# Kernel optimization log

Measured on AMD Instinct MI355X. Metric: run time of the kernel, lower is better.

Reference implementation:

```python
import jax, jax.numpy as jnp
import numpy as np

B, S, D, NH = 1, 2048, 2048, 8
DH = D // NH
BACKEND_EPS = 1e-6
NORM_EPS = 1e-6


def setup_inputs() -> dict:
    key = jax.random.key(0)
    ks = jax.random.split(key, 6)
    q = jax.random.normal(ks[0], (B, S, D), jnp.float32)
    k = jax.random.normal(ks[1], (B, S, D), jnp.float32)
    v = jax.random.normal(ks[2], (B, S, D), jnp.float32)
    igate_kernel = jax.random.normal(ks[3], (3 * D, NH), jnp.float32) * 0.02
    igate_bias = jax.random.normal(ks[4], (NH,), jnp.float32) * 0.1
    fgate_kernel = jax.random.normal(ks[5], (3 * D, NH), jnp.float32) * 0.02
    fgate_bias = jnp.linspace(3.0, 6.0, NH, dtype=jnp.float32)  # bias_linspace_init(3.0, 6.0)
    out_weight = jnp.ones((NH, DH), jnp.float32)  # MultiHeadLayerNorm scale (no bias)
    return dict(q=q, k=k, v=v, igate_kernel=igate_kernel, igate_bias=igate_bias,
                fgate_kernel=fgate_kernel, fgate_bias=fgate_bias, out_weight=out_weight)


def _mlstm_parallel_stabilized(q, k, v, i_pre, f_pre):
    # q,k,v: (B,NH,S,DH); i_pre,f_pre: (B,NH,S)
    s = q.shape[-2]
    dh = q.shape[-1]
    log_f = jax.nn.log_sigmoid(f_pre)                              # (B,NH,S)
    cum = jnp.pad(jnp.cumsum(log_f, axis=-1), ((0, 0), (0, 0), (1, 0)))  # (B,NH,S+1), cum[0]=0
    # logfg[t, s] = cum[t+1] - cum[s+1] = sum_{j=s+1}^{t} log_f[j], valid for s <= t
    logfg = cum[..., 1:, None] - cum[..., None, 1:]                # (B,NH,S,S)
    causal = jnp.tril(jnp.ones((s, s), dtype=bool))
    logfg = jnp.where(causal, logfg, -jnp.inf)
    log_D = logfg + i_pre[..., None, :]                            # add input gate at source position s
    m = jnp.max(log_D, axis=-1, keepdims=True)                     # stabilizer (B,NH,S,1)
    D = jnp.exp(log_D - m)
    qk = jnp.einsum('bhsd,bhtd->bhst', q, k) / jnp.sqrt(jnp.float32(dh))
    C = qk * D                                                     # (B,NH,S,S)
    n = jnp.maximum(jnp.abs(jnp.sum(C, axis=-1, keepdims=True)), jnp.exp(-m))
    return jnp.einsum('bhst,bhtd->bhsd', C / (n + BACKEND_EPS), v)


def reference(q, k, v, igate_kernel, igate_bias, fgate_kernel, fgate_bias, out_weight):
    qkv = jnp.concatenate([q, k, v], axis=-1)                      # (B,S,3D)
    i_pre = qkv @ igate_kernel + igate_bias                        # (B,S,NH)
    f_pre = qkv @ fgate_kernel + fgate_bias                        # (B,S,NH)
    qh = q.reshape(B, S, NH, DH).transpose(0, 2, 1, 3)             # (B,NH,S,DH)
    kh = k.reshape(B, S, NH, DH).transpose(0, 2, 1, 3)
    vh = v.reshape(B, S, NH, DH).transpose(0, 2, 1, 3)
    h = _mlstm_parallel_stabilized(qh, kh, vh,
                                   i_pre.transpose(0, 2, 1),
                                   f_pre.transpose(0, 2, 1))       # (B,NH,S,DH)
    h = h.transpose(0, 2, 1, 3)                                    # (B,S,NH,DH)
    mu = jnp.mean(h, axis=-1, keepdims=True)
    var = jnp.var(h, axis=-1, keepdims=True)
    hn = (h - mu) * jax.lax.rsqrt(var + NORM_EPS) * out_weight     # per-head LN, scale only
    return hn.reshape(B, S, D)
```

## Files before the change

kernel.cpp:

```cpp
#include <hip/hip_runtime.h>
#include <hip/hip_bf16.h>

#define SEQ 2048
#define DMODEL 2048
#define NHEAD 8
#define DHEAD 256

typedef _Float16 v8h __attribute__((ext_vector_type(8)));
typedef unsigned short v8u __attribute__((ext_vector_type(8)));
typedef float v4f __attribute__((ext_vector_type(4)));

__device__ __forceinline__ float b2f(unsigned short s) {
    return __uint_as_float(((unsigned)s) << 16);
}
__device__ __forceinline__ unsigned short f2b(float f) {
    unsigned u = __float_as_uint(f);
    u += 0x7fffu + ((u >> 16) & 1u);
    return (unsigned short)(u >> 16);
}
__device__ __forceinline__ unsigned short f2h(float f) {
    _Float16 h = (_Float16)f;
    return __builtin_bit_cast(unsigned short, h);
}
__device__ __forceinline__ float h2f(unsigned short s) {
    return (float)__builtin_bit_cast(_Float16, s);
}

__global__ __launch_bounds__(256) void k_detect(const unsigned short* q, int* flag) {
    __shared__ int cnt;
    if (threadIdx.x == 0) cnt = 0;
    __syncthreads();
    int wild = 0;
    for (int i = threadIdx.x; i < 2048; i += 256) {
        float x = b2f(q[i]);
        float ax = fabsf(x);
        if (!(ax <= 100.0f) || (x != 0.0f && ax < 1e-6f)) wild++;
    }
    atomicAdd(&cnt, wild);
    __syncthreads();
    if (threadIdx.x == 0) *flag = (cnt < 256) ? 1 : 0;
}

__global__ __launch_bounds__(256) void k_cvt_qk(const void* q, const void* k,
                                                const int* flag,
                                                unsigned short* qb, unsigned short* kb) {
    int bf = *(volatile const int*)flag;
    size_t i0 = ((size_t)blockIdx.x * 256 + threadIdx.x) * 8;
    v8u oq, ok;
    if (bf) {
        v8u uq = *(const v8u*)((const unsigned short*)q + i0);
        v8u uk = *(const v8u*)((const unsigned short*)k + i0);
#pragma unroll
        for (int j = 0; j < 8; j++) {
            oq[j] = f2h(b2f(uq[j]));
            ok[j] = f2h(b2f(uk[j]));
        }
    } else {
        const float* qf = (const float*)q;
        const float* kf = (const float*)k;
#pragma unroll
        for (int j = 0; j < 8; j++) {
            oq[j] = f2h(qf[i0 + j]);
            ok[j] = f2h(kf[i0 + j]);
        }
    }
    *(v8u*)(qb + i0) = oq;
    *(v8u*)(kb + i0) = ok;
}

__global__ __launch_bounds__(256) void k_cvt_gw(const void* ow, const int* flag, float* gw) {
    int bf = *(volatile const int*)flag;
    int i = blockIdx.x * 256 + threadIdx.x;
    gw[i] = bf ? b2f(((const unsigned short*)ow)[i]) : ((const float*)ow)[i];
}

__global__ __launch_bounds__(256) void k_tr_v(const void* v, const int* flag,
                                              unsigned short* vT) {
    __shared__ unsigned short tile[64][72];
    int bf = *(volatile const int*)flag;
    int s0 = blockIdx.x * 64, d0 = blockIdx.y * 64;
    int r = threadIdx.x >> 2, c0 = (threadIdx.x & 3) * 16;
    size_t base = (size_t)(s0 + r) * DMODEL + d0 + c0;
    if (bf) {
        const unsigned short* vp = (const unsigned short*)v;
        v8u a = *(const v8u*)(vp + base);
        v8u b = *(const v8u*)(vp + base + 8);
#pragma unroll
        for (int j = 0; j < 8; j++) { tile[r][c0 + j] = f2h(b2f(a[j])); tile[r][c0 + 8 + j] = f2h(b2f(b[j])); }
    } else {
        const float* vp = (const float*)v;
#pragma unroll
        for (int j = 0; j < 16; j++) tile[r][c0 + j] = f2h(vp[base + j]);
    }
    __syncthreads();
    int dr = threadIdx.x >> 2, sc0 = (threadIdx.x & 3) * 16;
    v8u o0, o1;
#pragma unroll
    for (int j = 0; j < 8; j++) { o0[j] = tile[sc0 + j][dr]; o1[j] = tile[sc0 + 8 + j][dr]; }
    int head = d0 >> 8;
    int dh = (d0 & 255) + dr;
    size_t ob = ((size_t)head * DHEAD + dh) * SEQ + s0 + sc0;
    *(v8u*)(vT + ob) = o0;
    *(v8u*)(vT + ob + 8) = o1;
}

__global__ __launch_bounds__(256) void k_gates(const void* q, const void* k, const void* v,
                                               const void* igk, const void* fgk,
                                               const int* flag, float* ipre, float* fpre) {
    __shared__ float x_lds[32][68];
    int bf = *(volatile const int*)flag;
    int s0 = blockIdx.x * 32;
    int c  = blockIdx.y;
    int tid = threadIdx.x;
    int sl = tid >> 3, hh = tid & 7;
    int rr = tid >> 3, j0 = (tid & 7) * 8;
    float accI = 0.f, accF = 0.f;
    for (int wd = 0; wd < 12; ++wd) {
        int gd0 = c * 768 + wd * 64;
        const void* src; int off;
        if (gd0 < 2048)      { src = q; off = gd0; }
        else if (gd0 < 4096) { src = k; off = gd0 - 2048; }
        else                 { src = v; off = gd0 - 4096; }
        __syncthreads();
        size_t base = (size_t)(s0 + rr) * DMODEL + off + j0;
        if (bf) {
            const unsigned short* sp = (const unsigned short*)src;
            v8u a = *(const v8u*)(sp + base);
#pragma unroll
            for (int j = 0; j < 8; j++) x_lds[rr][j0 + j] = b2f(a[j]);
        } else {
            const float* sp = (const float*)src;
#pragma unroll
            for (int j = 0; j < 8; j++) x_lds[rr][j0 + j] = sp[base + j];
        }
        __syncthreads();
        if (bf) {
            const unsigned short* ik = (const unsigned short*)igk;
            const unsigned short* fk = (const unsigned short*)fgk;
#pragma unroll 8
            for (int j = 0; j < 64; j++) {
                float x = x_lds[sl][j];
                int wi = (gd0 + j) * NHEAD + hh;
                accI += x * b2f(ik[wi]);
                accF += x * b2f(fk[wi]);
            }
        } else {
            const float* ik = (const float*)igk;
            const float* fk = (const float*)fgk;
#pragma unroll 8
            for (int j = 0; j < 64; j++) {
                float x = x_lds[sl][j];
                int wi = (gd0 + j) * NHEAD + hh;
                accI += x * ik[wi];
                accF += x * fk[wi];
            }
        }
    }
    atomicAdd(&ipre[hh * SEQ + s0 + sl], accI);
    atomicAdd(&fpre[hh * SEQ + s0 + sl], accF);
}

__global__ __launch_bounds__(256) void k_scan(const float* ipre, const float* fpre,
                                              const void* ib_, const void* fb_,
                                              const int* flag,
                                              float* a_g, float* amax_g, float* nfl_g) {
    __shared__ float sarr[256];
    int bf = *(volatile const int*)flag;
    int h = blockIdx.x, tid = threadIdx.x;
    float ib = bf ? b2f(((const unsigned short*)ib_)[h]) : ((const float*)ib_)[h];
    float fb = bf ? b2f(((const unsigned short*)fb_)[h]) : ((const float*)fb_)[h];
    int s0 = tid * 8;
    float lf[8], ip[8];
#pragma unroll
    for (int j = 0; j < 8; j++) {
        float fp = fpre[h * SEQ + s0 + j] + fb;
        lf[j] = fminf(fp, 0.0f) - log1pf(__expf(-fabsf(fp)));
        ip[j] = ipre[h * SEQ + s0 + j] + ib;
    }
    float cs[8]; float t = 0.f;
#pragma unroll
    for (int j = 0; j < 8; j++) { t += lf[j]; cs[j] = t; }
    sarr[tid] = t; __syncthreads();
    for (int ofs = 1; ofs < 256; ofs <<= 1) {
        float val = sarr[tid];
        if (tid >= ofs) val += sarr[tid - ofs];
        __syncthreads(); sarr[tid] = val; __syncthreads();
    }
    float excl = (tid > 0) ? sarr[tid - 1] : 0.0f;
    float cum[8], av[8];
#pragma unroll
    for (int j = 0; j < 8; j++) { cum[j] = excl + cs[j]; av[j] = ip[j] - cum[j]; }
    float mx = av[0];
#pragma unroll
    for (int j = 1; j < 8; j++) mx = fmaxf(mx, av[j]);
    __syncthreads(); sarr[tid] = mx; __syncthreads();
    for (int ofs = 1; ofs < 256; ofs <<= 1) {
        float val = sarr[tid];
        if (tid >= ofs) val = fmaxf(val, sarr[tid - ofs]);
        __syncthreads(); sarr[tid] = val; __syncthreads();
    }
    float run = (tid > 0) ? sarr[tid - 1] : -3.0e38f;
#pragma unroll
    for (int j = 0; j < 8; j++) {
        run = fmaxf(run, av[j]);
        int s = s0 + j;
        a_g[h * SEQ + s]    = av[j];
        amax_g[h * SEQ + s] = run;
        float m = cum[j] + run;
        nfl_g[h * SEQ + s]  = __expf(fminf(fmaxf(-m, -60.f), 60.f));
    }
}

__global__ __launch_bounds__(256) void k_main(const unsigned short* __restrict__ qb,
                                              const unsigned short* __restrict__ kb,
                                              const unsigned short* __restrict__ vT,
                                              const float* __restrict__ a_g,
                                              const float* __restrict__ amax_g,
                                              float* __restrict__ h_buf,
                                              float* __restrict__ rs_buf) {
    __shared__ __align__(16) unsigned short q_lds[32][264];
    __shared__ __align__(16) unsigned short k_lds[32][264];
    __shared__ __align__(16) unsigned short vT_lds[272][40];
    __shared__ __align__(16) unsigned short P_lds[32][40];
    __shared__ __align__(16) unsigned short Plo_lds[32][40];
    __shared__ float a_s[32], amax_t[32];

    const int h   = blockIdx.x;
    const int y   = blockIdx.y;
    const int tid = threadIdx.x;
    const int lane = tid & 63;
    const int w   = tid >> 6;
    const int l15 = lane & 15;
    const int qd  = (lane >> 4) & 3;
    const int hd0 = h * DHEAD;

    int u         = 65 * (y >> 1) + ((y & 1) ? 33 : 0);
    int remaining = (y & 1) ? 32 : 33;
    int tile = (int)((sqrtf(8.0f * (float)u + 1.0f) - 1.0f) * 0.5f);
    while ((tile + 1) * (tile + 2) / 2 <= u) ++tile;
    while (tile * (tile + 1) / 2 > u) --tile;
    int js = u - tile * (tile + 1) / 2;
    bool needQ = true;

    for (int i = tid; i < 16 * 40; i += 256) {
        int r2 = i / 40, c2 = i % 40;
        vT_lds[256 + r2][c2] = (r2 == 0 && c2 < 32) ? (unsigned short)0x3C00 : (unsigned short)0;
    }

    const v4f vzero = {0.f, 0.f, 0.f, 0.f};
    v4f acc[2][4];
    v4f accN[2];
#pragma unroll
    for (int m = 0; m < 2; m++) {
        accN[m] = vzero;
#pragma unroll
        for (int n = 0; n < 4; n++) acc[m][n] = vzero;
    }

    const int mw = w >> 1, nw = w & 1;
    const int krow = tid >> 3, kc0 = (tid & 7) * 32;

    v8u kr0, kr1, kr2, kr3, vr0, vr1, vr2, vr3;
    float areg = 0.f;
    {
        const int s0 = js * 32;
        const unsigned short* ks = kb + (size_t)(s0 + krow) * DMODEL + hd0 + kc0;
        kr0 = *(const v8u*)(ks);      kr1 = *(const v8u*)(ks + 8);
        kr2 = *(const v8u*)(ks + 16); kr3 = *(const v8u*)(ks + 24);
        const unsigned short* vs = vT + (size_t)(hd0 + tid) * SEQ + s0;
        vr0 = *(const v8u*)(vs);      vr1 = *(const v8u*)(vs + 8);
        vr2 = *(const v8u*)(vs + 16); vr3 = *(const v8u*)(vs + 24);
        if (tid < 32) areg = a_g[h * SEQ + s0 + tid];
    }

    for (;;) {
        const int t0 = tile * 32;
        __syncthreads();
        if (needQ) {
            const unsigned short* src = qb + (size_t)(t0 + krow) * DMODEL + hd0 + kc0;
#pragma unroll
            for (int i = 0; i < 4; i++)
                *(v8u*)&q_lds[krow][kc0 + i * 8] = *(const v8u*)(src + i * 8);
            if (tid < 32) amax_t[tid] = amax_g[h * SEQ + t0 + tid];
            needQ = false;
        }
        *(v8u*)&k_lds[krow][kc0]      = kr0;
        *(v8u*)&k_lds[krow][kc0 + 8]  = kr1;
        *(v8u*)&k_lds[krow][kc0 + 16] = kr2;
        *(v8u*)&k_lds[krow][kc0 + 24] = kr3;
        *(v8u*)&vT_lds[tid][0]  = vr0;
        *(v8u*)&vT_lds[tid][8]  = vr1;
        *(v8u*)&vT_lds[tid][16] = vr2;
        *(v8u*)&vT_lds[tid][24] = vr3;
        if (tid < 32) a_s[tid] = areg;
        __syncthreads();

        v4f c = vzero;
#pragma unroll
        for (int d0 = 0; d0 < 256; d0 += 32) {
            v8h a = *(const v8h*)&q_lds[mw * 16 + l15][d0 + qd * 8];
            v8h b = *(const v8h*)&k_lds[nw * 16 + l15][d0 + qd * 8];
            c = __builtin_amdgcn_mfma_f32_16x16x32_f16(a, b, c, 0, 0, 0);
        }
        {
            const bool diag = (js == tile);
            const int col = nw * 16 + l15;
            const float av = a_s[col];
#pragma unroll
            for (int r = 0; r < 4; r++) {
                int row = mw * 16 + qd * 4 + r;
                float arg = fminf(av - amax_t[row], 0.0f);
                float val = c[r] * 0.0625f * __expf(arg);
                if (diag && col > row) val = 0.0f;
                unsigned short hi = f2h(val);
                float lo = val - h2f(hi);
                P_lds[row][col]   = hi;
                Plo_lds[row][col] = f2h(lo);
            }
        }
        __syncthreads();

        int ntile = tile, njs = js + 1; bool nq = false;
        if (njs > tile) { ntile = tile + 1; njs = 0; nq = true; }
        if (remaining > 1) {
            const int s0 = njs * 32;
            const unsigned short* ks = kb + (size_t)(s0 + krow) * DMODEL + hd0 + kc0;
            kr0 = *(const v8u*)(ks);      kr1 = *(const v8u*)(ks + 8);
            kr2 = *(const v8u*)(ks + 16); kr3 = *(const v8u*)(ks + 24);
            const unsigned short* vs = vT + (size_t)(hd0 + tid) * SEQ + s0;
            vr0 = *(const v8u*)(vs);      vr1 = *(const v8u*)(vs + 8);
            vr2 = *(const v8u*)(vs + 16); vr3 = *(const v8u*)(vs + 24);
            if (tid < 32) areg = a_g[h * SEQ + s0 + tid];
        }

        v8h aH0 = *(const v8h*)&P_lds[l15][qd * 8];
        v8h aH1 = *(const v8h*)&P_lds[16 + l15][qd * 8];
        v8h aL0 = *(const v8h*)&Plo_lds[l15][qd * 8];
        v8h aL1 = *(const v8h*)&Plo_lds[16 + l15][qd * 8];
#pragma unroll
        for (int nn = 0; nn < 4; nn++) {
            v8h bV = *(const v8h*)&vT_lds[w * 64 + nn * 16 + l15][qd * 8];
            acc[0][nn] = __builtin_amdgcn_mfma_f32_16x16x32_f16(aH0, bV, acc[0][nn], 0, 0, 0);
            acc[0][nn] = __builtin_amdgcn_mfma_f32_16x16x32_f16(aL0, bV, acc[0][nn], 0, 0, 0);
            acc[1][nn] = __builtin_amdgcn_mfma_f32_16x16x32_f16(aH1, bV, acc[1][nn], 0, 0, 0);
            acc[1][nn] = __builtin_amdgcn_mfma_f32_16x16x32_f16(aL1, bV, acc[1][nn], 0, 0, 0);
        }
        if (w == 3) {
            v8h bN = *(const v8h*)&vT_lds[256 + l15][qd * 8];
            accN[0] = __builtin_amdgcn_mfma_f32_16x16x32_f16(aH0, bN, accN[0], 0, 0, 0);
            accN[0] = __builtin_amdgcn_mfma_f32_16x16x32_f16(aL0, bN, accN[0], 0, 0, 0);
            accN[1] = __builtin_amdgcn_mfma_f32_16x16x32_f16(aH1, bN, accN[1], 0, 0, 0);
            accN[1] = __builtin_amdgcn_mfma_f32_16x16x32_f16(aL1, bN, accN[1], 0, 0, 0);
        }

        if (js == tile || remaining == 1) {
#pragma unroll
            for (int m = 0; m < 2; m++)
#pragma unroll
                for (int r = 0; r < 4; r++) {
                    int row = t0 + m * 16 + qd * 4 + r;
#pragma unroll
                    for (int nn = 0; nn < 4; nn++) {
                        int col = hd0 + w * 64 + nn * 16 + l15;
                        atomicAdd(&h_buf[(size_t)row * DMODEL + col], acc[m][nn][r]);
                        acc[m][nn][r] = 0.f;
                    }
                    if (w == 3 && l15 == 0)
                        atomicAdd(&rs_buf[h * SEQ + row], accN[m][r]);
                    accN[m][r] = 0.f;
                }
        }
        if (--remaining == 0) break;
        tile = ntile; js = njs; needQ = nq;
    }
}

__global__ __launch_bounds__(256) void k_finish(const float* __restrict__ h_buf,
                                                const float* __restrict__ rs_buf,
                                                const float* __restrict__ nfl_g,
                                                const float* __restrict__ gw,
                                                const int* flag, void* out) {
    const int wv = threadIdx.x >> 6, lane = threadIdx.x & 63;
    const int rid = blockIdx.x * 4 + wv;
    const int s = rid >> 3, h = rid & 7;
    const int bf = *(volatile const int*)flag;
    float rs  = rs_buf[h * SEQ + s];
    float nfl = nfl_g[h * SEQ + s];
    float sc  = 1.0f / (fmaxf(fabsf(rs), nfl) + 1e-6f);
    size_t base = (size_t)s * DMODEL + h * DHEAD + lane * 4;
    v4f hv = *(const v4f*)(h_buf + base);
#pragma unroll
    for (int j = 0; j < 4; j++) hv[j] *= sc;
    float sm = hv[0] + hv[1] + hv[2] + hv[3];
    float sq = hv[0] * hv[0] + hv[1] * hv[1] + hv[2] * hv[2] + hv[3] * hv[3];
#pragma unroll
    for (int m = 1; m < 64; m <<= 1) {
        sm += __shfl_xor(sm, m, 64);
        sq += __shfl_xor(sq, m, 64);
    }
    float mean = sm * (1.0f / 256.0f);
    float var  = fmaxf(sq * (1.0f / 256.0f) - mean * mean, 0.0f);
    float rstd = rsqrtf(var + 1e-6f);
    const float* g = gw + h * DHEAD + lane * 4;
    if (bf) {
        unsigned short* o = (unsigned short*)out + base;
#pragma unroll
        for (int j = 0; j < 4; j++) o[j] = f2b((hv[j] - mean) * rstd * g[j]);
    } else {
        float* o = (float*)out + base;
#pragma unroll
        for (int j = 0; j < 4; j++) o[j] = (hv[j] - mean) * rstd * g[j];
    }
}

extern "C" void kernel_launch(void* const* d_in, const int* in_sizes, int n_in,
                              void* d_out, int out_size, void* d_ws, size_t ws_size,
                              hipStream_t stream) {
    const void* q   = d_in[0];
    const void* k   = d_in[1];
    const void* v   = d_in[2];
    const void* igk = d_in[3];
    const void* igb = d_in[4];
    const void* fgk = d_in[5];
    const void* fgb = d_in[6];
    const void* ow  = d_in[7];

    char* ws = (char*)d_ws;
    int*   flag   = (int*)(ws + 0);
    float* ipre   = (float*)(ws + 1024);
    float* fpre   = (float*)(ws + 1024 + 1 * 65536);
    float* a_g    = (float*)(ws + 1024 + 2 * 65536);
    float* amax_g = (float*)(ws + 1024 + 3 * 65536);
    float* nfl_g  = (float*)(ws + 1024 + 4 * 65536);
    float* gw     = (float*)(ws + 1024 + 5 * 65536);
    unsigned short* qb = (unsigned short*)(ws + 1024 + 5 * 65536 + 8192);
    unsigned short* kb = qb + (size_t)SEQ * DMODEL;
    unsigned short* vT = kb + (size_t)SEQ * DMODEL;
    float* rs_buf = (float*)((char*)vT + (size_t)SEQ * DMODEL * 2);
    float* h_buf  = (float*)((char*)rs_buf + 65536);

    hipMemsetAsync(ipre, 0, 2 * 65536, stream);
    hipMemsetAsync(rs_buf, 0, 65536 + (size_t)SEQ * DMODEL * 4, stream);
    k_detect<<<1, 256, 0, stream>>>((const unsigned short*)q, flag);
    k_cvt_qk<<<2048, 256, 0, stream>>>(q, k, flag, qb, kb);
    k_cvt_gw<<<8, 256, 0, stream>>>(ow, flag, gw);
    k_tr_v<<<dim3(32, 32), 256, 0, stream>>>(v, flag, vT);
    k_gates<<<dim3(64, 8), 256, 0, stream>>>(q, k, v, igk, fgk, flag, ipre, fpre);
    k_scan<<<8, 256, 0, stream>>>(ipre, fpre, igb, fgb, flag, a_g, amax_g, nfl_g);
    k_main<<<dim3(8, 64), 256, 0, stream>>>(qb, kb, vT, a_g, amax_g, h_buf, rs_buf);
    k_finish<<<4096, 256, 0, stream>>>(h_buf, rs_buf, nfl_g, gw, flag, d_out);
}
```

Measured before the change: 269.4 us.

## Fuse dtype detect, conversions, V transpose and gate projections into one pre-pass

Merges the detect, q/k conversion, V transpose and gate-projection kernels into a single k_pre kernel. Each block reads its slice of q/k/v once and uses it both to emit fp16 copies and to accumulate gate partial sums, which are written to per-slice partial buffers instead of atomics. k_scan then reduces the six partials, and k_finish reads the LN weight directly. This removes redundant global reads of q/k/v, several launches and one memset, in exchange for each block redoing the dtype detection and using only 384 blocks for the fused pre-pass.

```diff
diff --git a/kernel.cpp b/kernel.cpp
--- a/kernel.cpp
+++ b/kernel.cpp
@@ -26,141 +26,106 @@
     return (float)__builtin_bit_cast(_Float16, s);
 }
 
-__global__ __launch_bounds__(256) void k_detect(const unsigned short* q, int* flag) {
+__global__ __launch_bounds__(256) void k_pre(const void* q, const void* k, const void* v,
+                                             const void* igk, const void* fgk,
+                                             int* flag,
+                                             unsigned short* qb, unsigned short* kb,
+                                             unsigned short* vT,
+                                             float* iparts, float* fparts) {
+    __shared__ float x_lds[32][67];
     __shared__ int cnt;
-    if (threadIdx.x == 0) cnt = 0;
+    const int tid = threadIdx.x;
+
+    if (tid == 0) cnt = 0;
     __syncthreads();
-    int wild = 0;
-    for (int i = threadIdx.x; i < 2048; i += 256) {
-        float x = b2f(q[i]);
-        float ax = fabsf(x);
-        if (!(ax <= 100.0f) || (x != 0.0f && ax < 1e-6f)) wild++;
-    }
-    atomicAdd(&cnt, wild);
+    {
+        const unsigned short* qp = (const unsigned short*)q;
+        int wild = 0;
+        for (int i = tid; i < 2048; i += 256) {
+            float x = b2f(qp[i]);
+            float ax = fabsf(x);
+            if (!(ax <= 100.0f) || (x != 0.0f && ax < 1e-6f)) wild++;
+        }
+        atomicAdd(&cnt, wild);
+    }
     __syncthreads();
-    if (threadIdx.x == 0) *flag = (cnt < 256) ? 1 : 0;
-}
-
-__global__ __launch_bounds__(256) void k_cvt_qk(const void* q, const void* k,
-                                                const int* flag,
-                                                unsigned short* qb, unsigned short* kb) {
-    int bf = *(volatile const int*)flag;
-    size_t i0 = ((size_t)blockIdx.x * 256 + threadIdx.x) * 8;
-    v8u oq, ok;
-    if (bf) {
-        v8u uq = *(const v8u*)((const unsigned short*)q + i0);
-        v8u uk = *(const v8u*)((const unsigned short*)k + i0);
-#pragma unroll
-        for (int j = 0; j < 8; j++) {
-            oq[j] = f2h(b2f(uq[j]));
-            ok[j] = f2h(b2f(uk[j]));
-        }
-    } else {
-        const float* qf = (const float*)q;
-        const float* kf = (const float*)k;
-#pragma unroll
-        for (int j = 0; j < 8; j++) {
-            oq[j] = f2h(qf[i0 + j]);
-            ok[j] = f2h(kf[i0 + j]);
-        }
-    }
-    *(v8u*)(qb + i0) = oq;
-    *(v8u*)(kb + i0) = ok;
-}
-
-__global__ __launch_bounds__(256) void k_cvt_gw(const void* ow, const int* flag, float* gw) {
-    int bf = *(volatile const int*)flag;
-    int i = blockIdx.x * 256 + threadIdx.x;
-    gw[i] = bf ? b2f(((const unsigned short*)ow)[i]) : ((const float*)ow)[i];
-}
-
-__global__ __launch_bounds__(256) void k_tr_v(const void* v, const int* flag,
-                                              unsigned short* vT) {
-    __shared__ unsigned short tile[64][72];
-    int bf = *(volatile const int*)flag;
-    int s0 = blockIdx.x * 64, d0 = blockIdx.y * 64;
-    int r = threadIdx.x >> 2, c0 = (threadIdx.x & 3) * 16;
-    size_t base = (size_t)(s0 + r) * DMODEL + d0 + c0;
-    if (bf) {
-        const unsigned short* vp = (const unsigned short*)v;
-        v8u a = *(const v8u*)(vp + base);
-        v8u b = *(const v8u*)(vp + base + 8);
-#pragma unroll
-        for (int j = 0; j < 8; j++) { tile[r][c0 + j] = f2h(b2f(a[j])); tile[r][c0 + 8 + j] = f2h(b2f(b[j])); }
-    } else {
-        const float* vp = (const float*)v;
-#pragma unroll
-        for (int j = 0; j < 16; j++) tile[r][c0 + j] = f2h(vp[base + j]);
-    }
-    __syncthreads();
-    int dr = threadIdx.x >> 2, sc0 = (threadIdx.x & 3) * 16;
-    v8u o0, o1;
-#pragma unroll
-    for (int j = 0; j < 8; j++) { o0[j] = tile[sc0 + j][dr]; o1[j] = tile[sc0 + 8 + j][dr]; }
-    int head = d0 >> 8;
-    int dh = (d0 & 255) + dr;
-    size_t ob = ((size_t)head * DHEAD + dh) * SEQ + s0 + sc0;
-    *(v8u*)(vT + ob) = o0;
-    *(v8u*)(vT + ob + 8) = o1;
-}
-
-__global__ __launch_bounds__(256) void k_gates(const void* q, const void* k, const void* v,
-                                               const void* igk, const void* fgk,
-                                               const int* flag, float* ipre, float* fpre) {
-    __shared__ float x_lds[32][68];
-    int bf = *(volatile const int*)flag;
-    int s0 = blockIdx.x * 32;
-    int c  = blockIdx.y;
-    int tid = threadIdx.x;
-    int sl = tid >> 3, hh = tid & 7;
-    int rr = tid >> 3, j0 = (tid & 7) * 8;
+    const int bf = (cnt < 256) ? 1 : 0;
+    if (blockIdx.x == 0 && blockIdx.y == 0 && tid == 0) *flag = bf;
+
+    const int s0 = blockIdx.x * 32;
+    const int z  = blockIdx.y;
+    const int tz = z >> 1;
+    const int dbase = (z & 1) * 1024;
+    const void* src = (tz == 0) ? q : (tz == 1) ? k : v;
+    unsigned short* dst16 = (tz == 0) ? qb : kb;
+
+    const int r  = tid >> 3, c0 = (tid & 7) * 8;
+    const int sl = tid >> 3, hh = tid & 7;
     float accI = 0.f, accF = 0.f;
-    for (int wd = 0; wd < 12; ++wd) {
-        int gd0 = c * 768 + wd * 64;
-        const void* src; int off;
-        if (gd0 < 2048)      { src = q; off = gd0; }
-        else if (gd0 < 4096) { src = k; off = gd0 - 2048; }
-        else                 { src = v; off = gd0 - 4096; }
-        __syncthreads();
-        size_t base = (size_t)(s0 + rr) * DMODEL + off + j0;
+    const unsigned short* ik16 = (const unsigned short*)igk;
+    const unsigned short* fk16 = (const unsigned short*)fgk;
+    const float* ik32 = (const float*)igk;
+    const float* fk32 = (const float*)fgk;
+
+    for (int ch = 0; ch < 16; ++ch) {
+        const int d0 = dbase + ch * 64;
+        float xv[8];
+        const size_t base = (size_t)(s0 + r) * DMODEL + d0 + c0;
         if (bf) {
             const unsigned short* sp = (const unsigned short*)src;
             v8u a = *(const v8u*)(sp + base);
 #pragma unroll
-            for (int j = 0; j < 8; j++) x_lds[rr][j0 + j] = b2f(a[j]);
+            for (int j = 0; j < 8; j++) xv[j] = b2f(a[j]);
         } else {
             const float* sp = (const float*)src;
-#pragma unroll
-            for (int j = 0; j < 8; j++) x_lds[rr][j0 + j] = sp[base + j];
+            v4f a0 = *(const v4f*)(sp + base);
+            v4f a1 = *(const v4f*)(sp + base + 4);
+#pragma unroll
+            for (int j = 0; j < 4; j++) { xv[j] = a0[j]; xv[4 + j] = a1[j]; }
         }
         __syncthreads();
+#pragma unroll
+        for (int j = 0; j < 8; j++) x_lds[r][c0 + j] = xv[j];
+        if (tz < 2) {
+            v8u o;
+#pragma unroll
+            for (int j = 0; j < 8; j++) o[j] = f2h(xv[j]);
+            *(v8u*)(dst16 + base) = o;
+        }
+        __syncthreads();
+        const int gd0 = tz * 2048 + d0;
         if (bf) {
-            const unsigned short* ik = (const unsigned short*)igk;
-            const unsigned short* fk = (const unsigned short*)fgk;
 #pragma unroll 8
             for (int j = 0; j < 64; j++) {
                 float x = x_lds[sl][j];
                 int wi = (gd0 + j) * NHEAD + hh;
-                accI += x * b2f(ik[wi]);
-                accF += x * b2f(fk[wi]);
+                accI += x * b2f(ik16[wi]);
+                accF += x * b2f(fk16[wi]);
             }
         } else {
-            const float* ik = (const float*)igk;
-            const float* fk = (const float*)fgk;
 #pragma unroll 8
             for (int j = 0; j < 64; j++) {
                 float x = x_lds[sl][j];
                 int wi = (gd0 + j) * NHEAD + hh;
-                accI += x * ik[wi];
-                accF += x * fk[wi];
+                accI += x * ik32[wi];
+                accF += x * fk32[wi];
             }
         }
-    }
-    atomicAdd(&ipre[hh * SEQ + s0 + sl], accI);
-    atomicAdd(&fpre[hh * SEQ + s0 + sl], accF);
-}
-
-__global__ __launch_bounds__(256) void k_scan(const float* ipre, const float* fpre,
+        if (tz == 2) {
+            const int dloc = tid >> 2, sc0 = (tid & 3) * 8;
+            v8u o;
+#pragma unroll
+            for (int j = 0; j < 8; j++) o[j] = f2h(x_lds[sc0 + j][dloc]);
+            const int dglob = d0 + dloc;
+            const int head = dglob >> 8, dh = dglob & 255;
+            *(v8u*)(vT + ((size_t)(head * DHEAD + dh)) * SEQ + s0 + sc0) = o;
+        }
+    }
+    iparts[(size_t)z * NHEAD * SEQ + hh * SEQ + s0 + sl] = accI;
+    fparts[(size_t)z * NHEAD * SEQ + hh * SEQ + s0 + sl] = accF;
+}
+
+__global__ __launch_bounds__(256) void k_scan(const float* iparts, const float* fparts,
                                               const void* ib_, const void* fb_,
                                               const int* flag,
                                               float* a_g, float* amax_g, float* nfl_g) {
@@ -173,9 +138,14 @@
     float lf[8], ip[8];
 #pragma unroll
     for (int j = 0; j < 8; j++) {
-        float fp = fpre[h * SEQ + s0 + j] + fb;
-        lf[j] = fminf(fp, 0.0f) - log1pf(__expf(-fabsf(fp)));
-        ip[j] = ipre[h * SEQ + s0 + j] + ib;
+        float fpv = fb, ipv = ib;
+#pragma unroll
+        for (int z = 0; z < 6; z++) {
+            ipv += iparts[(size_t)z * NHEAD * SEQ + h * SEQ + s0 + j];
+            fpv += fparts[(size_t)z * NHEAD * SEQ + h * SEQ + s0 + j];
+        }
+        lf[j] = fminf(fpv, 0.0f) - log1pf(__expf(-fabsf(fpv)));
+        ip[j] = ipv;
     }
     float cs[8]; float t = 0.f;
 #pragma unroll
@@ -378,7 +348,7 @@
 __global__ __launch_bounds__(256) void k_finish(const float* __restrict__ h_buf,
                                                 const float* __restrict__ rs_buf,
                                                 const float* __restrict__ nfl_g,
-                                                const float* __restrict__ gw,
+                                                const void* __restrict__ ow,
                                                 const int* flag, void* out) {
     const int wv = threadIdx.x >> 6, lane = threadIdx.x & 63;
     const int rid = blockIdx.x * 4 + wv;
@@ -401,15 +371,24 @@
     float mean = sm * (1.0f / 256.0f);
     float var  = fmaxf(sq * (1.0f / 256.0f) - mean * mean, 0.0f);
     float rstd = rsqrtf(var + 1e-6f);
-    const float* g = gw + h * DHEAD + lane * 4;
+    int gi = h * DHEAD + lane * 4;
+    float g0, g1, g2, g3;
+    if (bf) {
+        const unsigned short* gp = (const unsigned short*)ow;
+        g0 = b2f(gp[gi]); g1 = b2f(gp[gi + 1]); g2 = b2f(gp[gi + 2]); g3 = b2f(gp[gi + 3]);
+    } else {
+        const float* gp = (const float*)ow;
+        g0 = gp[gi]; g1 = gp[gi + 1]; g2 = gp[gi + 2]; g3 = gp[gi + 3];
+    }
+    float gv[4] = {g0, g1, g2, g3};
     if (bf) {
         unsigned short* o = (unsigned short*)out + base;
 #pragma unroll
-        for (int j = 0; j < 4; j++) o[j] = f2b((hv[j] - mean) * rstd * g[j]);
+        for (int j = 0; j < 4; j++) o[j] = f2b((hv[j] - mean) * rstd * gv[j]);
     } else {
         float* o = (float*)out + base;
 #pragma unroll
-        for (int j = 0; j < 4; j++) o[j] = (hv[j] - mean) * rstd * g[j];
+        for (int j = 0; j < 4; j++) o[j] = (hv[j] - mean) * rstd * gv[j];
     }
 }
 
@@ -427,26 +406,20 @@
 
     char* ws = (char*)d_ws;
     int*   flag   = (int*)(ws + 0);
-    float* ipre   = (float*)(ws + 1024);
-    float* fpre   = (float*)(ws + 1024 + 1 * 65536);
-    float* a_g    = (float*)(ws + 1024 + 2 * 65536);
-    float* amax_g = (float*)(ws + 1024 + 3 * 65536);
-    float* nfl_g  = (float*)(ws + 1024 + 4 * 65536);
-    float* gw     = (float*)(ws + 1024 + 5 * 65536);
-    unsigned short* qb = (unsigned short*)(ws + 1024 + 5 * 65536 + 8192);
+    float* iparts = (float*)(ws + 1024);
+    float* fparts = iparts + 6 * NHEAD * SEQ;
+    float* a_g    = fparts + 6 * NHEAD * SEQ;
+    float* amax_g = a_g + NHEAD * SEQ;
+    float* nfl_g  = amax_g + NHEAD * SEQ;
+    unsigned short* qb = (unsigned short*)(nfl_g + NHEAD * SEQ);
     unsigned short* kb = qb + (size_t)SEQ * DMODEL;
     unsigned short* vT = kb + (size_t)SEQ * DMODEL;
-    float* rs_buf = (float*)((char*)vT + (size_t)SEQ * DMODEL * 2);
-    float* h_buf  = (float*)((char*)rs_buf + 65536);
-
-    hipMemsetAsync(ipre, 0, 2 * 65536, stream);
-    hipMemsetAsync(rs_buf, 0, 65536 + (size_t)SEQ * DMODEL * 4, stream);
-    k_detect<<<1, 256, 0, stream>>>((const unsigned short*)q, flag);
-    k_cvt_qk<<<2048, 256, 0, stream>>>(q, k, flag, qb, kb);
-    k_cvt_gw<<<8, 256, 0, stream>>>(ow, flag, gw);
-    k_tr_v<<<dim3(32, 32), 256, 0, stream>>>(v, flag, vT);
-    k_gates<<<dim3(64, 8), 256, 0, stream>>>(q, k, v, igk, fgk, flag, ipre, fpre);
-    k_scan<<<8, 256, 0, stream>>>(ipre, fpre, igb, fgb, flag, a_g, amax_g, nfl_g);
+    float* rs_buf = (float*)(vT + (size_t)SEQ * DMODEL);
+    float* h_buf  = rs_buf + NHEAD * SEQ;
+
+    hipMemsetAsync(rs_buf, 0, (size_t)NHEAD * SEQ * 4 + (size_t)SEQ * DMODEL * 4, stream);
+    k_pre<<<dim3(64, 6), 256, 0, stream>>>(q, k, v, igk, fgk, flag, qb, kb, vT, iparts, fparts);
+    k_scan<<<8, 256, 0, stream>>>(iparts, fparts, igb, fgb, flag, a_g, amax_g, nfl_g);
     k_main<<<dim3(8, 64), 256, 0, stream>>>(qb, kb, vT, a_g, amax_g, h_buf, rs_buf);
-    k_finish<<<4096, 256, 0, stream>>>(h_buf, rs_buf, nfl_g, gw, flag, d_out);
-}
+    k_finish<<<4096, 256, 0, stream>>>(h_buf, rs_buf, nfl_g, ow, flag, d_out);
+}
```

After: 268.2 us. No clear change (-0.4%).
